# Optimization experiments

Measured on AMD Instinct MI355X. Metric: run time of the kernel, lower is better.

Reference implementation:

```python
import jax, jax.numpy as jnp
import numpy as np

HIDDEN = 1024
HEADS = 16
DEPTH = HIDDEN // HEADS  # 64
B, S = 1, 2048  # batch must be 1: E is built with shape (heads, B*S, depth) and the skew reshape assumes B*S == S


def setup_inputs() -> dict:
    key = jax.random.key(0)
    ks = jax.random.split(key, 6)
    std = 0.02
    x = jax.random.normal(ks[0], (B, S, HIDDEN), dtype=jnp.float32)
    c_attn_w = jax.random.normal(ks[1], (HIDDEN, 3 * HIDDEN), dtype=jnp.float32) * std
    c_attn_b = jnp.zeros((1, 3 * HIDDEN), dtype=jnp.float32)
    c_proj_w = jax.random.normal(ks[2], (HIDDEN, HIDDEN), dtype=jnp.float32) * std
    c_proj_b = jnp.zeros((1, HIDDEN), dtype=jnp.float32)
    # GlorotUniform for E of shape (heads, B*S, depth)
    limit = float(np.sqrt(6.0 / (B * S + DEPTH)))
    E = jax.random.uniform(ks[3], (HEADS, B * S, DEPTH), dtype=jnp.float32,
                           minval=-limit, maxval=limit)
    return {"x": x, "c_attn_w": c_attn_w, "c_attn_b": c_attn_b,
            "c_proj_w": c_proj_w, "c_proj_b": c_proj_b, "E": E}


def _split_heads(t):
    # [B,S,H] -> [B,heads,S,depth]
    b, s, h = t.shape
    return t.reshape(b, s, HEADS, h // HEADS).transpose(0, 2, 1, 3)


def _relative_attention(q, E):
    # Transformer-XL style skewing. q: [B,heads,S,depth], E: [heads,B*S,depth]
    b, h, s, d = q.shape
    q_ = q.transpose(1, 0, 2, 3).reshape(h, b * s, d)
    rel = jnp.einsum('hnd,hmd->hnm', q_, E)            # [h, B*S, B*S]
    rel = rel.reshape(h, b, s, s)
    rel = jnp.pad(rel, ((0, 0), (0, 0), (0, 0), (1, 0)))  # pad left on last dim
    rel = rel.reshape(h, b, s + 1, s)[:, :, 1:]            # skew
    return rel.transpose(1, 0, 2, 3)                       # [B,heads,S,S]


def reference(x, c_attn_w, c_attn_b, c_proj_w, c_proj_b, E):
    b, s, hidden = x.shape
    qkv = x @ c_attn_w + c_attn_b                      # [B,S,3H]
    q, k, v = jnp.split(qkv, 3, axis=2)
    q, k, v = _split_heads(q), _split_heads(k), _split_heads(v)  # [B,h,S,d]

    w = jnp.einsum('bhqd,bhkd->bhqk', q, k)            # raw scores
    w = w + _relative_attention(q, E)
    w = w * jax.lax.rsqrt(jnp.asarray(DEPTH, w.dtype))  # scale applied after rel bias

    # causal mask: 1 in lower triangle (i >= j - ns + nd, nd == ns == S)
    i = jnp.arange(s)[:, None]
    j = jnp.arange(s)[None, :]
    bmask = (i >= j).astype(w.dtype)[None, None]        # [1,1,S,S]
    w = w * bmask - 10000.0 * (1.0 - bmask)

    a = jax.nn.softmax(w, axis=-1)                      # dropout is identity at inference
    ctx = jnp.einsum('bhqk,bhkd->bhqd', a, v)
    ctx = ctx.transpose(0, 2, 1, 3).reshape(b, s, hidden)  # merge heads
    out = ctx @ c_proj_w + c_proj_b
    return out
```

## Files before the change

### kernel.cpp

```cpp
#include <hip/hip_runtime.h>
#include <math.h>

#define SEQ  2048
#define NH   16
#define DEP  64
#define HID  1024

typedef __attribute__((ext_vector_type(8))) short s16x8;
typedef __attribute__((ext_vector_type(4))) float f32x4;

#define MFMA16(a, b, c) __builtin_amdgcn_mfma_f32_16x16x32_bf16(a, b, c, 0, 0, 0)
#define GLDS16(g, l)                                                           \
  __builtin_amdgcn_global_load_lds(                                            \
      (const __attribute__((address_space(1))) void*)(g),                      \
      (__attribute__((address_space(3))) void*)(l), 16, 0, 0)

__device__ __forceinline__ ushort f2b(float f) {
  union { float f; unsigned u; } x; x.f = f;
  unsigned r = (x.u + 0x7fff + ((x.u >> 16) & 1)) >> 16;
  return (ushort)r;
}
__device__ __forceinline__ float b2f(ushort u) {
  union { unsigned u; float f; } x; x.u = ((unsigned)u) << 16;
  return x.f;
}

__global__ __launch_bounds__(256) void prep(
    const float* __restrict__ x, ushort* __restrict__ xb,
    const float* __restrict__ E, ushort* __restrict__ Eb,
    const float* __restrict__ Wa, ushort* __restrict__ Wat,
    const float* __restrict__ Wp, ushort* __restrict__ Wpt) {
  const int bid = blockIdx.x, t = threadIdx.x;
  if (bid < 1024) {
    __shared__ float Ls[64 * 68];
    const float* in; ushort* out; int C, tile;
    if (bid < 768) { in = Wa; out = Wat; C = 3072; tile = bid; }
    else           { in = Wp; out = Wpt; C = 1024; tile = bid - 768; }
    const int ntx = C / 64;
    const int n0 = (tile % ntx) * 64, k0 = (tile / ntx) * 64;
    const int r = t >> 4, c4 = t & 15;
    #pragma unroll
    for (int p = 0; p < 4; p++) {
      float4 v = *(const float4*)&in[(size_t)(k0 + r + 16 * p) * C + n0 + c4 * 4];
      *(float4*)&Ls[(r + 16 * p) * 68 + c4 * 4] = v;
    }
    __syncthreads();
    #pragma unroll
    for (int p = 0; p < 4; p++) {
      int rw = r + 16 * p;
      ushort4 o;
      o.x = f2b(Ls[(c4 * 4 + 0) * 68 + rw]);
      o.y = f2b(Ls[(c4 * 4 + 1) * 68 + rw]);
      o.z = f2b(Ls[(c4 * 4 + 2) * 68 + rw]);
      o.w = f2b(Ls[(c4 * 4 + 3) * 68 + rw]);
      *(ushort4*)&out[(size_t)(n0 + rw) * 1024 + k0 + c4 * 4] = o;
    }
  } else {
    const int id = bid - 1024;
    #pragma unroll
    for (int rep = 0; rep < 4; rep++) {
      int i = id * 256 + t + rep * 262144;
      const float* src; ushort* dst; int k;
      if (i < 524288) { src = x; dst = xb; k = i; }
      else            { src = E; dst = Eb; k = i - 524288; }
      float4 v = *(const float4*)&src[(size_t)k * 4];
      ushort4 o = {f2b(v.x), f2b(v.y), f2b(v.z), f2b(v.w)};
      *(ushort4*)&dst[(size_t)k * 4] = o;
    }
  }
}

template <int MODE>
__global__ __launch_bounds__(256, 3) void gemm_mfma(
    const ushort* __restrict__ A, const ushort* __restrict__ Bt,
    const float* __restrict__ bias, int N, int K,
    ushort* __restrict__ qd, ushort* __restrict__ kd, ushort* __restrict__ vt,
    float* __restrict__ Cout) {
  __shared__ ushort As[2][64 * 64];
  __shared__ ushort Bs[2][128 * 64];
  const int t = threadIdx.x, l = t & 63, w = t >> 6;
  const int lr = l & 15, quad = l >> 4;
  const int row8 = l >> 3;
  const int chunk = (l & 7) ^ ((l >> 3) & 7);
  const int m0 = blockIdx.y * 64, n0 = blockIdx.x * 128;
  const int wr = (w >> 1) * 32, wc = (w & 1) * 64;
  f32x4 acc[2][4] = {};
  const ushort* gA = A + (size_t)m0 * K + chunk * 8;
  const ushort* gB = Bt + (size_t)n0 * K + chunk * 8;

  auto issue = [&](int buf, int k0) {
    #pragma unroll
    for (int g = 0; g < 2; g++) {
      int r = 16 * w + 8 * g + row8;
      GLDS16(gA + (size_t)r * K + k0, &As[buf][(16 * w + 8 * g) * 64]);
    }
    #pragma unroll
    for (int g = 0; g < 4; g++) {
      int r = 32 * w + 8 * g + row8;
      GLDS16(gB + (size_t)r * K + k0, &Bs[buf][(32 * w + 8 * g) * 64]);
    }
  };

  issue(0, 0);
  const int nsteps = K / 64;
  for (int s = 0; s < nsteps; s++) {
    __syncthreads();
    if (s + 1 < nsteps) issue((s + 1) & 1, (s + 1) * 64);
    const char* as_ = (const char*)As[s & 1];
    const char* bs_ = (const char*)Bs[s & 1];
    s16x8 af[2][2], bf[4][2];
    #pragma unroll
    for (int i = 0; i < 2; i++)
      #pragma unroll
      for (int hh = 0; hh < 2; hh++)
        af[i][hh] = *(const s16x8*)(as_ + (wr + 16 * i + lr) * 128 +
                                    (((4 * hh + quad) ^ (lr & 7)) * 16));
    #pragma unroll
    for (int j = 0; j < 4; j++)
      #pragma unroll
      for (int hh = 0; hh < 2; hh++)
        bf[j][hh] = *(const s16x8*)(bs_ + (wc + 16 * j + lr) * 128 +
                                    (((4 * hh + quad) ^ (lr & 7)) * 16));
    #pragma unroll
    for (int i = 0; i < 2; i++)
      #pragma unroll
      for (int j = 0; j < 4; j++) {
        acc[i][j] = MFMA16(af[i][0], bf[j][0], acc[i][j]);
        acc[i][j] = MFMA16(af[i][1], bf[j][1], acc[i][j]);
      }
  }

  #pragma unroll
  for (int i = 0; i < 2; i++) {
    #pragma unroll
    for (int j = 0; j < 4; j++) {
      const int colg = n0 + wc + 16 * j + lr;
      const float bb = bias[colg];
      const int rowg0 = m0 + wr + 16 * i + 4 * quad;
      if (MODE == 0) {
        const int part = colg >> 10, hh = (colg >> 6) & 15, d = colg & 63;
        if (part == 2) {
          ushort4 ov;
          ov.x = f2b(acc[i][j][0] + bb);
          ov.y = f2b(acc[i][j][1] + bb);
          ov.z = f2b(acc[i][j][2] + bb);
          ov.w = f2b(acc[i][j][3] + bb);
          *(ushort4*)&vt[((size_t)hh * 64 + d) * SEQ + rowg0] = ov;
        } else {
          ushort* dst = part == 0 ? qd : kd;
          const float sc = part == 0 ? 0.125f : 1.0f;
          #pragma unroll
          for (int r = 0; r < 4; r++)
            dst[((size_t)hh * SEQ + rowg0 + r) * 64 + d] = f2b((acc[i][j][r] + bb) * sc);
        }
      } else {
        #pragma unroll
        for (int r = 0; r < 4; r++)
          Cout[(size_t)(rowg0 + r) * N + colg] = acc[i][j][r] + bb;
      }
    }
  }
}

__global__ __launch_bounds__(256, 2) void attn_mfma(
    const ushort* __restrict__ qw, const ushort* __restrict__ kw,
    const ushort* __restrict__ vT, const ushort* __restrict__ Ebf,
    ushort* __restrict__ ctx, ushort* __restrict__ pa_o,
    float* __restrict__ pa_l) {
  __shared__ ushort KT[2][64 * 64];
  __shared__ ushort VS[2][64 * 64];
  __shared__ ushort EB[2][128 * 64];
  __shared__ ushort PB[4][16 * 72];
  const int t = threadIdx.x, l = t & 63, w = t >> 6;
  const int lr = l & 15, quad = l >> 4;
  const int row8 = l >> 3;
  const int chunk = (l & 7) ^ ((l >> 3) & 7);
  const int h = blockIdx.y;
  const int p = blockIdx.x >> 1, half = blockIdx.x & 1;
  const int i0A = 64 * p, i0B = 64 * (31 - p);

  int ph_i0[2], ph_k0[2], ph_k1[2], nph, tot;
  bool ph_diag[2], ph_dir[2];
  if (half == 0) {
    ph_i0[0] = i0A; ph_k0[0] = 0; ph_k1[0] = p + 1;  ph_diag[0] = true;  ph_dir[0] = true;
    ph_i0[1] = i0B; ph_k0[1] = 0; ph_k1[1] = 16 - p; ph_diag[1] = false; ph_dir[1] = false;
    nph = 2; tot = 17;
  } else {
    ph_i0[0] = i0B; ph_k0[0] = 16 - p; ph_k1[0] = 32 - p; ph_diag[0] = true; ph_dir[0] = false;
    ph_i0[1] = 0; ph_k0[1] = 0; ph_k1[1] = 0; ph_diag[1] = false; ph_dir[1] = false;
    nph = 1; tot = 16;
  }

  const ushort* kwh = kw + (size_t)h * SEQ * 64;
  const ushort* vgh = vT + (size_t)h * 64 * SEQ;
  const ushort* egh = Ebf + (size_t)h * SEQ * 64;

  auto issue = [&](int buf, int i0_, int j0) {
    const int m0 = 1984 - i0_ + j0;
    const ushort* kb = kwh + (size_t)j0 * 64 + chunk * 8;
    const ushort* vb = vgh + j0 + chunk * 8;
    #pragma unroll
    for (int g = 0; g < 2; g++) {
      int r = 16 * w + 8 * g + row8;
      GLDS16(kb + (size_t)r * 64, &KT[buf][(16 * w + 8 * g) * 64]);
      GLDS16(vb + (size_t)r * SEQ, &VS[buf][(16 * w + 8 * g) * 64]);
    }
    #pragma unroll
    for (int g = 0; g < 4; g++) {
      int r = m0 + 32 * w + 8 * g + row8;
      if (r > SEQ - 1) r = SEQ - 1;
      GLDS16(egh + (size_t)r * 64 + chunk * 8, &EB[buf][(32 * w + 8 * g) * 64]);
    }
  };

  int pi = 0, kt = ph_k0[0];
  issue(0, ph_i0[0], kt * 64);

  s16x8 aq0, aq1;
  {
    const ushort* qg = qw + ((size_t)h * SEQ + ph_i0[0] + 16 * w) * 64;
    aq0 = *(const s16x8*)(qg + lr * 64 + quad * 8);
    aq1 = *(const s16x8*)(qg + lr * 64 + 32 + quad * 8);
  }

  f32x4 o[4] = {};
  float li[4] = {0.f, 0.f, 0.f, 0.f};
  f32x4 rtc = {};

  for (int s = 0; s < tot; s++) {
    __syncthreads();

    const int i0 = ph_i0[pi];
    const bool first = (kt == ph_k0[pi]);
    const bool last = (kt == ph_k1[pi] - 1);
    const bool diag = ph_diag[pi] && last;

    {
      int npi = pi, nkt = kt + 1;
      bool have = true;
      if (nkt == ph_k1[pi]) {
        if (pi + 1 < nph) { npi = pi + 1; nkt = ph_k0[npi]; } else have = false;
      }
      if (have) issue((s + 1) & 1, ph_i0[npi], nkt * 64);
    }

    const char* KTc = (const char*)KT[s & 1];
    const char* VSc = (const char*)VS[s & 1];
    const char* EBc = (const char*)EB[s & 1];

    f32x4 s4[4];
    #pragma unroll
    for (int b = 0; b < 4; b++) {
      const int row = 16 * b + lr;
      s16x8 bk0 = *(const s16x8*)(KTc + row * 128 + ((quad ^ (lr & 7)) * 16));
      s16x8 bk1 = *(const s16x8*)(KTc + row * 128 + (((4 + quad) ^ (lr & 7)) * 16));
      f32x4 z = {};
      z = MFMA16(aq0, bk0, z);
      z = MFMA16(aq1, bk1, z);
      s4[b] = z;
    }

    {
      const int ebase = 48 - 16 * w;
      f32x4 rt[5];
      if (first) {
        const int row = ebase + lr;
        s16x8 e0 = *(const s16x8*)(EBc + row * 128 + ((quad ^ (lr & 7)) * 16));
        s16x8 e1 = *(const s16x8*)(EBc + row * 128 + (((4 + quad) ^ (lr & 7)) * 16));
        f32x4 z = {};
        z = MFMA16(aq0, e0, z);
        z = MFMA16(aq1, e1, z);
        rt[0] = z;
      } else {
        rt[0] = rtc;
      }
      #pragma unroll
      for (int b = 1; b < 5; b++) {
        const int row = ebase + 16 * b + lr;
        s16x8 e0 = *(const s16x8*)(EBc + row * 128 + ((quad ^ (lr & 7)) * 16));
        s16x8 e1 = *(const s16x8*)(EBc + row * 128 + (((4 + quad) ^ (lr & 7)) * 16));
        f32x4 z = {};
        z = MFMA16(aq0, e0, z);
        z = MFMA16(aq1, e1, z);
        rt[b] = z;
      }
      rtc = rt[4];
      #pragma unroll
      for (int b = 0; b < 4; b++)
        #pragma unroll
        for (int r = 0; r < 4; r++) {
          int ti = 4 * quad + r;
          int u = lr - ti + 15;
          int src = (u & 15) | (l & 48);
          float v0 = __shfl(rt[b][r], src);
          float v1 = __shfl(rt[b + 1][r], src);
          s4[b][r] += (u < 16) ? v0 : v1;
        }
    }

    if (diag) {
      #pragma unroll
      for (int b = 0; b < 4; b++)
        #pragma unroll
        for (int r = 0; r < 4; r++) {
          int ii = 16 * w + 4 * quad + r;
          if (16 * b + lr > ii) s4[b][r] = -10000.0f;
        }
    }

    #pragma unroll
    for (int b = 0; b < 4; b++)
      #pragma unroll
      for (int r = 0; r < 4; r++) {
        float pp = __expf(s4[b][r]);
        s4[b][r] = pp;
        li[r] += pp;
      }

    {
      char* Pw = (char*)PB[w];
      #pragma unroll
      for (int b = 0; b < 4; b++)
        #pragma unroll
        for (int r = 0; r < 4; r++)
          *(ushort*)(Pw + (4 * quad + r) * 144 + (16 * b + lr) * 2) = f2b(s4[b][r]);
      s16x8 pa0 = *(const s16x8*)(Pw + lr * 144 + quad * 16);
      s16x8 pa1 = *(const s16x8*)(Pw + lr * 144 + 64 + quad * 16);
      #pragma unroll
      for (int dc = 0; dc < 4; dc++) {
        const int row = 16 * dc + lr;
        s16x8 bv0 = *(const s16x8*)(VSc + row * 128 + ((quad ^ (lr & 7)) * 16));
        s16x8 bv1 = *(const s16x8*)(VSc + row * 128 + (((4 + quad) ^ (lr & 7)) * 16));
        o[dc] = MFMA16(pa0, bv0, o[dc]);
        o[dc] = MFMA16(pa1, bv1, o[dc]);
      }
    }

    if (last) {
      float lsum[4];
      #pragma unroll
      for (int r = 0; r < 4; r++) {
        float v = li[r];
        v += __shfl_xor(v, 1);
        v += __shfl_xor(v, 2);
        v += __shfl_xor(v, 4);
        v += __shfl_xor(v, 8);
        lsum[r] = v;
      }
      if (ph_dir[pi]) {
        #pragma unroll
        for (int r = 0; r < 4; r++) {
          float inv = 1.0f / lsum[r];
          #pragma unroll
          for (int dc = 0; dc < 4; dc++) {
            int row = i0 + 16 * w + 4 * quad + r;
            int col = h * 64 + 16 * dc + lr;
            ctx[(size_t)row * HID + col] = f2b(o[dc][r] * inv);
          }
        }
      } else {
        ushort* po = pa_o + (((size_t)(h * 16 + p) * 2 + half) * 4096);
        float* pl = pa_l + (((size_t)(h * 16 + p) * 2 + half) * 64);
        #pragma unroll
        for (int r = 0; r < 4; r++) {
          int row = 16 * w + 4 * quad + r;
          #pragma unroll
          for (int dc = 0; dc < 4; dc++)
            po[row * 64 + 16 * dc + lr] = f2b(o[dc][r]);
          if (lr == 0) pl[row] = lsum[r];
        }
      }
      #pragma unroll
      for (int dc = 0; dc < 4; dc++) o[dc] = (f32x4){0.f, 0.f, 0.f, 0.f};
      #pragma unroll
      for (int r = 0; r < 4; r++) li[r] = 0.f;
      if (pi + 1 < nph) {
        const ushort* qg = qw + ((size_t)h * SEQ + ph_i0[pi + 1] + 16 * w) * 64;
        aq0 = *(const s16x8*)(qg + lr * 64 + quad * 8);
        aq1 = *(const s16x8*)(qg + lr * 64 + 32 + quad * 8);
      }
    }

    if (kt + 1 == ph_k1[pi]) { pi++; kt = (pi < nph) ? ph_k0[pi] : 0; }
    else kt++;
  }
}

__global__ __launch_bounds__(256) void merge_p(const ushort* __restrict__ pa_o,
                                               const float* __restrict__ pa_l,
                                               ushort* __restrict__ ctx) {
  const int p = blockIdx.x, h = blockIdx.y, t = threadIdx.x;
  const int row = t >> 2, seg = t & 3;
  const ushort* o0 = pa_o + ((size_t)(h * 16 + p) * 2 + 0) * 4096;
  const ushort* o1 = pa_o + ((size_t)(h * 16 + p) * 2 + 1) * 4096;
  const float* l0 = pa_l + ((size_t)(h * 16 + p) * 2 + 0) * 64;
  const float* l1 = pa_l + ((size_t)(h * 16 + p) * 2 + 1) * 64;
  const float inv = 1.0f / (l0[row] + l1[row]);
  const int i0b = 64 * (31 - p);
  #pragma unroll
  for (int g = 0; g < 2; g++) {
    ushort a[8], b[8], r[8];
    *(int4*)a = *(const int4*)&o0[row * 64 + seg * 16 + g * 8];
    *(int4*)b = *(const int4*)&o1[row * 64 + seg * 16 + g * 8];
    #pragma unroll
    for (int j = 0; j < 8; j++) r[j] = f2b((b2f(a[j]) + b2f(b[j])) * inv);
    *(int4*)&ctx[(size_t)(i0b + row) * HID + h * 64 + seg * 16 + g * 8] = *(int4*)r;
  }
}

extern "C" void kernel_launch(void* const* d_in, const int* in_sizes, int n_in,
                              void* d_out, int out_size, void* d_ws, size_t ws_size,
                              hipStream_t stream) {
  (void)in_sizes; (void)n_in; (void)out_size; (void)ws_size;
  const float* x  = (const float*)d_in[0];
  const float* Wa = (const float*)d_in[1];
  const float* ba = (const float*)d_in[2];
  const float* Wp = (const float*)d_in[3];
  const float* bp = (const float*)d_in[4];
  const float* E  = (const float*)d_in[5];
  float* out = (float*)d_out;

  ushort* xb  = (ushort*)d_ws;
  ushort* ctx = xb;
  ushort* Wat = xb + (size_t)2 * 1024 * 1024;
  ushort* Wpt = Wat + (size_t)3 * 1024 * 1024;
  ushort* Ebf = Wpt + (size_t)1024 * 1024;
  ushort* qwp = Ebf + (size_t)2 * 1024 * 1024;
  ushort* kwp = qwp + (size_t)2 * 1024 * 1024;
  ushort* vTp = kwp + (size_t)2 * 1024 * 1024;
  ushort* pa_o = Wat;
  float*  pa_l = (float*)(Wat + (size_t)2 * 1024 * 1024);

  prep<<<2048, 256, 0, stream>>>(x, xb, E, Ebf, Wa, Wat, Wp, Wpt);
  gemm_mfma<0><<<dim3(24, 32), 256, 0, stream>>>(xb, Wat, ba, 3 * HID, HID,
                                                 qwp, kwp, vTp, nullptr);
  attn_mfma<<<dim3(32, NH), 256, 0, stream>>>(qwp, kwp, vTp, Ebf, ctx,
                                              pa_o, pa_l);
  merge_p<<<dim3(16, NH), 256, 0, stream>>>(pa_o, pa_l, ctx);
  gemm_mfma<1><<<dim3(8, 32), 256, 0, stream>>>(ctx, Wpt, bp, HID, HID,
                                                nullptr, nullptr, nullptr, out);
}
```

Before: 158.5 us.

## Use 128-row query tiles with 4-way split-K attention and ring-buffered E rows

```diff
diff --git a/kernel.cpp b/kernel.cpp
--- a/kernel.cpp
+++ b/kernel.cpp
@@ -70,21 +70,22 @@
   }
 }
 
-template <int MODE>
+template <int MODE, int BN>
 __global__ __launch_bounds__(256, 3) void gemm_mfma(
     const ushort* __restrict__ A, const ushort* __restrict__ Bt,
     const float* __restrict__ bias, int N, int K,
     ushort* __restrict__ qd, ushort* __restrict__ kd, ushort* __restrict__ vt,
     float* __restrict__ Cout) {
+  constexpr int NJ = BN / 32;
   __shared__ ushort As[2][64 * 64];
-  __shared__ ushort Bs[2][128 * 64];
+  __shared__ ushort Bs[2][BN * 64];
   const int t = threadIdx.x, l = t & 63, w = t >> 6;
   const int lr = l & 15, quad = l >> 4;
   const int row8 = l >> 3;
   const int chunk = (l & 7) ^ ((l >> 3) & 7);
-  const int m0 = blockIdx.y * 64, n0 = blockIdx.x * 128;
-  const int wr = (w >> 1) * 32, wc = (w & 1) * 64;
-  f32x4 acc[2][4] = {};
+  const int m0 = blockIdx.y * 64, n0 = blockIdx.x * BN;
+  const int wr = (w >> 1) * 32, wc = (w & 1) * (BN / 2);
+  f32x4 acc[2][NJ] = {};
   const ushort* gA = A + (size_t)m0 * K + chunk * 8;
   const ushort* gB = Bt + (size_t)n0 * K + chunk * 8;
 
@@ -95,9 +96,9 @@
       GLDS16(gA + (size_t)r * K + k0, &As[buf][(16 * w + 8 * g) * 64]);
     }
     #pragma unroll
-    for (int g = 0; g < 4; g++) {
-      int r = 32 * w + 8 * g + row8;
-      GLDS16(gB + (size_t)r * K + k0, &Bs[buf][(32 * w + 8 * g) * 64]);
+    for (int g = 0; g < BN / 32; g++) {
+      int r = (BN / 4) * w + 8 * g + row8;
+      GLDS16(gB + (size_t)r * K + k0, &Bs[buf][((BN / 4) * w + 8 * g) * 64]);
     }
   };
 
@@ -108,7 +109,7 @@
     if (s + 1 < nsteps) issue((s + 1) & 1, (s + 1) * 64);
     const char* as_ = (const char*)As[s & 1];
     const char* bs_ = (const char*)Bs[s & 1];
-    s16x8 af[2][2], bf[4][2];
+    s16x8 af[2][2], bf[NJ][2];
     #pragma unroll
     for (int i = 0; i < 2; i++)
       #pragma unroll
@@ -116,7 +117,7 @@
         af[i][hh] = *(const s16x8*)(as_ + (wr + 16 * i + lr) * 128 +
                                     (((4 * hh + quad) ^ (lr & 7)) * 16));
     #pragma unroll
-    for (int j = 0; j < 4; j++)
+    for (int j = 0; j < NJ; j++)
       #pragma unroll
       for (int hh = 0; hh < 2; hh++)
         bf[j][hh] = *(const s16x8*)(bs_ + (wc + 16 * j + lr) * 128 +
@@ -124,7 +125,7 @@
     #pragma unroll
     for (int i = 0; i < 2; i++)
       #pragma unroll
-      for (int j = 0; j < 4; j++) {
+      for (int j = 0; j < NJ; j++) {
         acc[i][j] = MFMA16(af[i][0], bf[j][0], acc[i][j]);
         acc[i][j] = MFMA16(af[i][1], bf[j][1], acc[i][j]);
       }
@@ -133,7 +134,7 @@
   #pragma unroll
   for (int i = 0; i < 2; i++) {
     #pragma unroll
-    for (int j = 0; j < 4; j++) {
+    for (int j = 0; j < NJ; j++) {
       const int colg = n0 + wc + 16 * j + lr;
       const float bb = bias[colg];
       const int rowg0 = m0 + wr + 16 * i + 4 * quad;
@@ -165,247 +166,249 @@
 __global__ __launch_bounds__(256, 2) void attn_mfma(
     const ushort* __restrict__ qw, const ushort* __restrict__ kw,
     const ushort* __restrict__ vT, const ushort* __restrict__ Ebf,
-    ushort* __restrict__ ctx, ushort* __restrict__ pa_o,
-    float* __restrict__ pa_l) {
+    ushort* __restrict__ pa_o, float* __restrict__ pa_l) {
   __shared__ ushort KT[2][64 * 64];
   __shared__ ushort VS[2][64 * 64];
-  __shared__ ushort EB[2][128 * 64];
-  __shared__ ushort PB[4][16 * 72];
+  __shared__ ushort EB[4][64 * 64];
+  __shared__ ushort PB[4][1152];
   const int t = threadIdx.x, l = t & 63, w = t >> 6;
   const int lr = l & 15, quad = l >> 4;
   const int row8 = l >> 3;
-  const int chunk = (l & 7) ^ ((l >> 3) & 7);
+  const int chk = (l & 7) ^ ((l >> 3) & 7);
   const int h = blockIdx.y;
-  const int p = blockIdx.x >> 1, half = blockIdx.x & 1;
-  const int i0A = 64 * p, i0B = 64 * (31 - p);
-
-  int ph_i0[2], ph_k0[2], ph_k1[2], nph, tot;
-  bool ph_diag[2], ph_dir[2];
-  if (half == 0) {
-    ph_i0[0] = i0A; ph_k0[0] = 0; ph_k1[0] = p + 1;  ph_diag[0] = true;  ph_dir[0] = true;
-    ph_i0[1] = i0B; ph_k0[1] = 0; ph_k1[1] = 16 - p; ph_diag[1] = false; ph_dir[1] = false;
-    nph = 2; tot = 17;
-  } else {
-    ph_i0[0] = i0B; ph_k0[0] = 16 - p; ph_k1[0] = 32 - p; ph_diag[0] = true; ph_dir[0] = false;
-    ph_i0[1] = 0; ph_k0[1] = 0; ph_k1[1] = 0; ph_diag[1] = false; ph_dir[1] = false;
-    nph = 1; tot = 16;
-  }
+  const int pr = blockIdx.x >> 2, cid = blockIdx.x & 3;
+  const int TA = 2 * pr + 2;
+  const int s0 = (17 * cid) >> 1, s1 = (17 * (cid + 1)) >> 1;
+  const int iA = 128 * pr, iB = 128 * (15 - pr);
 
   const ushort* kwh = kw + (size_t)h * SEQ * 64;
   const ushort* vgh = vT + (size_t)h * 64 * SEQ;
   const ushort* egh = Ebf + (size_t)h * SEQ * 64;
 
-  auto issue = [&](int buf, int i0_, int j0) {
-    const int m0 = 1984 - i0_ + j0;
-    const ushort* kb = kwh + (size_t)j0 * 64 + chunk * 8;
-    const ushort* vb = vgh + j0 + chunk * 8;
+  auto issueKV = [&](int buf, int j0) {
     #pragma unroll
     for (int g = 0; g < 2; g++) {
       int r = 16 * w + 8 * g + row8;
-      GLDS16(kb + (size_t)r * 64, &KT[buf][(16 * w + 8 * g) * 64]);
-      GLDS16(vb + (size_t)r * SEQ, &VS[buf][(16 * w + 8 * g) * 64]);
-    }
-    #pragma unroll
-    for (int g = 0; g < 4; g++) {
-      int r = m0 + 32 * w + 8 * g + row8;
-      if (r > SEQ - 1) r = SEQ - 1;
-      GLDS16(egh + (size_t)r * 64 + chunk * 8, &EB[buf][(32 * w + 8 * g) * 64]);
+      GLDS16(kwh + (size_t)(j0 + r) * 64 + chk * 8, &KT[buf][(16 * w + 8 * g) * 64]);
+      GLDS16(vgh + (size_t)r * SEQ + j0 + chk * 8, &VS[buf][(16 * w + 8 * g) * 64]);
     }
   };
-
-  int pi = 0, kt = ph_k0[0];
-  issue(0, ph_i0[0], kt * 64);
-
-  s16x8 aq0, aq1;
-  {
-    const ushort* qg = qw + ((size_t)h * SEQ + ph_i0[0] + 16 * w) * 64;
-    aq0 = *(const s16x8*)(qg + lr * 64 + quad * 8);
-    aq1 = *(const s16x8*)(qg + lr * 64 + 32 + quad * 8);
-  }
-
-  f32x4 o[4] = {};
-  float li[4] = {0.f, 0.f, 0.f, 0.f};
-  f32x4 rtc = {};
-
-  for (int s = 0; s < tot; s++) {
+  auto issueE = [&](int G) {
+    const int slot = (G >> 6) & 3;
+    #pragma unroll
+    for (int g = 0; g < 2; g++) {
+      int rl = 16 * w + 8 * g + row8;
+      int grow = G + rl; if (grow > SEQ - 1) grow = SEQ - 1;
+      GLDS16(egh + (size_t)grow * 64 + chk * 8, &EB[slot][(16 * w + 8 * g) * 64]);
+    }
+  };
+  auto eread = [&](int P, int h2) -> s16x8 {
+    int rg = P + lr;
+    return *(const s16x8*)((const char*)EB + ((rg >> 6) & 3) * 8192 +
+                           (rg & 63) * 128 + (((h2 * 4 + quad) ^ (lr & 7)) * 16));
+  };
+
+  int s = s0;
+  int i0 = (s0 < TA) ? iA : iB;
+  int tau = (s0 < TA) ? pr : 15 - pr;
+  int kt = (s0 < TA) ? s0 : s0 - TA;
+
+  s16x8 aq[2][2];
+  auto loadQ = [&]() {
+    const ushort* qg = qw + ((size_t)h * SEQ + i0 + 32 * w) * 64;
+    #pragma unroll
+    for (int a = 0; a < 2; a++)
+      #pragma unroll
+      for (int h2 = 0; h2 < 2; h2++)
+        aq[a][h2] = *(const s16x8*)(qg + (16 * a + lr) * 64 + h2 * 32 + quad * 8);
+  };
+  loadQ();
+
+  int MB = 1920 - i0 + 64 * kt;
+  issueE(MB); issueE(MB + 64); issueE(MB + 128);
+  issueKV(0, 64 * kt);
+
+  f32x4 o[2][4] = {};
+  float li[2][4] = {};
+  f32x4 rt0[5], rt1[5];
+  bool first = true, efill = false;
+
+  for (; s < s1; s++) {
     __syncthreads();
-
-    const int i0 = ph_i0[pi];
-    const bool first = (kt == ph_k0[pi]);
-    const bool last = (kt == ph_k1[pi] - 1);
-    const bool diag = ph_diag[pi] && last;
-
-    {
-      int npi = pi, nkt = kt + 1;
-      bool have = true;
-      if (nkt == ph_k1[pi]) {
-        if (pi + 1 < nph) { npi = pi + 1; nkt = ph_k0[npi]; } else have = false;
-      }
-      if (have) issue((s + 1) & 1, ph_i0[npi], nkt * 64);
-    }
-
-    const char* KTc = (const char*)KT[s & 1];
-    const char* VSc = (const char*)VS[s & 1];
-    const char* EBc = (const char*)EB[s & 1];
-
-    f32x4 s4[4];
+    if (efill) {
+      issueE(MB); issueE(MB + 64); issueE(MB + 128);
+      __syncthreads();
+      efill = false;
+    }
+
+    const int j0 = 64 * kt;
+    const bool lastOfPhase = (s + 1 == TA) || (s + 1 == s1);
+    if (s + 1 < s1) {
+      if (s + 1 == TA) issueKV((s + 1 - s0) & 1, 0);
+      else { issueKV((s + 1 - s0) & 1, j0 + 64); issueE(MB + 192); }
+    }
+
+    const char* KTc = (const char*)KT[(s - s0) & 1];
+    const char* VSc = (const char*)VS[(s - s0) & 1];
+
+    f32x4 s4[2][4];
     #pragma unroll
     for (int b = 0; b < 4; b++) {
       const int row = 16 * b + lr;
       s16x8 bk0 = *(const s16x8*)(KTc + row * 128 + ((quad ^ (lr & 7)) * 16));
       s16x8 bk1 = *(const s16x8*)(KTc + row * 128 + (((4 + quad) ^ (lr & 7)) * 16));
-      f32x4 z = {};
-      z = MFMA16(aq0, bk0, z);
-      z = MFMA16(aq1, bk1, z);
-      s4[b] = z;
+      f32x4 z0 = {}, z1 = {};
+      z0 = MFMA16(aq[0][0], bk0, z0); z0 = MFMA16(aq[0][1], bk1, z0);
+      z1 = MFMA16(aq[1][0], bk0, z1); z1 = MFMA16(aq[1][1], bk1, z1);
+      s4[0][b] = z0; s4[1][b] = z1;
     }
 
     {
-      const int ebase = 48 - 16 * w;
-      f32x4 rt[5];
+      const int base = MB + 112 - 32 * w;
       if (first) {
-        const int row = ebase + lr;
-        s16x8 e0 = *(const s16x8*)(EBc + row * 128 + ((quad ^ (lr & 7)) * 16));
-        s16x8 e1 = *(const s16x8*)(EBc + row * 128 + (((4 + quad) ^ (lr & 7)) * 16));
-        f32x4 z = {};
-        z = MFMA16(aq0, e0, z);
-        z = MFMA16(aq1, e1, z);
-        rt[0] = z;
-      } else {
-        rt[0] = rtc;
-      }
-      #pragma unroll
-      for (int b = 1; b < 5; b++) {
-        const int row = ebase + 16 * b + lr;
-        s16x8 e0 = *(const s16x8*)(EBc + row * 128 + ((quad ^ (lr & 7)) * 16));
-        s16x8 e1 = *(const s16x8*)(EBc + row * 128 + (((4 + quad) ^ (lr & 7)) * 16));
-        f32x4 z = {};
-        z = MFMA16(aq0, e0, z);
-        z = MFMA16(aq1, e1, z);
-        rt[b] = z;
-      }
-      rtc = rt[4];
+        s16x8 e0 = eread(base - 16, 0), e1 = eread(base - 16, 1);
+        f32x4 z = {}; z = MFMA16(aq[1][0], e0, z); z = MFMA16(aq[1][1], e1, z);
+        rt1[0] = z;
+      } else { rt0[0] = rt0[4]; rt1[0] = rt1[4]; }
+      #pragma unroll
+      for (int m = 0; m < 5; m++) {
+        s16x8 e0 = eread(base + 16 * m, 0), e1 = eread(base + 16 * m, 1);
+        if (m >= 1) {
+          f32x4 z = {}; z = MFMA16(aq[0][0], e0, z); z = MFMA16(aq[0][1], e1, z);
+          rt0[m] = z;
+        }
+        if (m <= 3) {
+          f32x4 z = {}; z = MFMA16(aq[1][0], e0, z); z = MFMA16(aq[1][1], e1, z);
+          rt1[m + 1] = z;
+        }
+        if (first && m == 0) {
+          f32x4 z = {}; z = MFMA16(aq[0][0], e0, z); z = MFMA16(aq[0][1], e1, z);
+          rt0[0] = z;
+        }
+      }
+    }
+    #pragma unroll
+    for (int b = 0; b < 4; b++)
+      #pragma unroll
+      for (int r = 0; r < 4; r++) {
+        const int ti = 4 * quad + r;
+        const int u = lr - ti + 15;
+        const int src = (u & 15) | (l & 48);
+        float v00 = __shfl(rt0[b][r], src), v01 = __shfl(rt0[b + 1][r], src);
+        float v10 = __shfl(rt1[b][r], src), v11 = __shfl(rt1[b + 1][r], src);
+        s4[0][b][r] += (u < 16) ? v00 : v01;
+        s4[1][b][r] += (u < 16) ? v10 : v11;
+      }
+
+    #pragma unroll
+    for (int a = 0; a < 2; a++) {
+      if (j0 + 63 > i0 + 32 * w + 16 * a) {
+        #pragma unroll
+        for (int b = 0; b < 4; b++)
+          #pragma unroll
+          for (int r = 0; r < 4; r++) {
+            int ii = i0 + 32 * w + 16 * a + 4 * quad + r;
+            int jj = j0 + 16 * b + lr;
+            if (jj > ii) s4[a][b][r] = -10000.0f;
+          }
+      }
+    }
+
+    #pragma unroll
+    for (int a = 0; a < 2; a++)
       #pragma unroll
       for (int b = 0; b < 4; b++)
         #pragma unroll
         for (int r = 0; r < 4; r++) {
-          int ti = 4 * quad + r;
-          int u = lr - ti + 15;
-          int src = (u & 15) | (l & 48);
-          float v0 = __shfl(rt[b][r], src);
-          float v1 = __shfl(rt[b + 1][r], src);
-          s4[b][r] += (u < 16) ? v0 : v1;
-        }
-    }
-
-    if (diag) {
-      #pragma unroll
-      for (int b = 0; b < 4; b++)
-        #pragma unroll
-        for (int r = 0; r < 4; r++) {
-          int ii = 16 * w + 4 * quad + r;
-          if (16 * b + lr > ii) s4[b][r] = -10000.0f;
-        }
-    }
-
-    #pragma unroll
-    for (int b = 0; b < 4; b++)
-      #pragma unroll
-      for (int r = 0; r < 4; r++) {
-        float pp = __expf(s4[b][r]);
-        s4[b][r] = pp;
-        li[r] += pp;
-      }
-
-    {
-      char* Pw = (char*)PB[w];
-      #pragma unroll
-      for (int b = 0; b < 4; b++)
-        #pragma unroll
-        for (int r = 0; r < 4; r++)
-          *(ushort*)(Pw + (4 * quad + r) * 144 + (16 * b + lr) * 2) = f2b(s4[b][r]);
-      s16x8 pa0 = *(const s16x8*)(Pw + lr * 144 + quad * 16);
-      s16x8 pa1 = *(const s16x8*)(Pw + lr * 144 + 64 + quad * 16);
+          float pp = __expf(s4[a][b][r]);
+          s4[a][b][r] = pp;
+          li[a][r] += pp;
+        }
+
+    char* Pw = (char*)PB + w * 2304;
+    #pragma unroll
+    for (int hc = 0; hc < 2; hc++) {
+      #pragma unroll
+      for (int a = 0; a < 2; a++)
+        #pragma unroll
+        for (int bb = 0; bb < 2; bb++)
+          #pragma unroll
+          for (int r = 0; r < 4; r++)
+            *(ushort*)(Pw + (16 * a + 4 * quad + r) * 72 + (16 * bb + lr) * 2) =
+                f2b(s4[a][2 * hc + bb][r]);
+      s16x8 pa0 = *(const s16x8*)(Pw + lr * 72 + quad * 16);
+      s16x8 pa1 = *(const s16x8*)(Pw + (16 + lr) * 72 + quad * 16);
       #pragma unroll
       for (int dc = 0; dc < 4; dc++) {
         const int row = 16 * dc + lr;
-        s16x8 bv0 = *(const s16x8*)(VSc + row * 128 + ((quad ^ (lr & 7)) * 16));
-        s16x8 bv1 = *(const s16x8*)(VSc + row * 128 + (((4 + quad) ^ (lr & 7)) * 16));
-        o[dc] = MFMA16(pa0, bv0, o[dc]);
-        o[dc] = MFMA16(pa1, bv1, o[dc]);
-      }
-    }
-
-    if (last) {
-      float lsum[4];
-      #pragma unroll
-      for (int r = 0; r < 4; r++) {
-        float v = li[r];
-        v += __shfl_xor(v, 1);
-        v += __shfl_xor(v, 2);
-        v += __shfl_xor(v, 4);
-        v += __shfl_xor(v, 8);
-        lsum[r] = v;
-      }
-      if (ph_dir[pi]) {
+        s16x8 bv = *(const s16x8*)(VSc + row * 128 + (((hc * 4 + quad) ^ (lr & 7)) * 16));
+        o[0][dc] = MFMA16(pa0, bv, o[0][dc]);
+        o[1][dc] = MFMA16(pa1, bv, o[1][dc]);
+      }
+    }
+
+    if (lastOfPhase) {
+      ushort* po = pa_o + (size_t)((h * 16 + tau) * 4 + cid) * 8192;
+      float* pl = pa_l + (size_t)((h * 16 + tau) * 4 + cid) * 128;
+      #pragma unroll
+      for (int a = 0; a < 2; a++)
         #pragma unroll
         for (int r = 0; r < 4; r++) {
-          float inv = 1.0f / lsum[r];
-          #pragma unroll
-          for (int dc = 0; dc < 4; dc++) {
-            int row = i0 + 16 * w + 4 * quad + r;
-            int col = h * 64 + 16 * dc + lr;
-            ctx[(size_t)row * HID + col] = f2b(o[dc][r] * inv);
-          }
-        }
-      } else {
-        ushort* po = pa_o + (((size_t)(h * 16 + p) * 2 + half) * 4096);
-        float* pl = pa_l + (((size_t)(h * 16 + p) * 2 + half) * 64);
-        #pragma unroll
-        for (int r = 0; r < 4; r++) {
-          int row = 16 * w + 4 * quad + r;
+          float v = li[a][r];
+          v += __shfl_xor(v, 1); v += __shfl_xor(v, 2);
+          v += __shfl_xor(v, 4); v += __shfl_xor(v, 8);
+          const int row = 32 * w + 16 * a + 4 * quad + r;
+          if (lr == 0) pl[row] = v;
           #pragma unroll
           for (int dc = 0; dc < 4; dc++)
-            po[row * 64 + 16 * dc + lr] = f2b(o[dc][r]);
-          if (lr == 0) pl[row] = lsum[r];
-        }
-      }
-      #pragma unroll
-      for (int dc = 0; dc < 4; dc++) o[dc] = (f32x4){0.f, 0.f, 0.f, 0.f};
-      #pragma unroll
-      for (int r = 0; r < 4; r++) li[r] = 0.f;
-      if (pi + 1 < nph) {
-        const ushort* qg = qw + ((size_t)h * SEQ + ph_i0[pi + 1] + 16 * w) * 64;
-        aq0 = *(const s16x8*)(qg + lr * 64 + quad * 8);
-        aq1 = *(const s16x8*)(qg + lr * 64 + 32 + quad * 8);
-      }
-    }
-
-    if (kt + 1 == ph_k1[pi]) { pi++; kt = (pi < nph) ? ph_k0[pi] : 0; }
-    else kt++;
+            po[row * 64 + 16 * dc + lr] = f2b(o[a][dc][r]);
+          li[a][r] = 0.f;
+        }
+      #pragma unroll
+      for (int a = 0; a < 2; a++)
+        #pragma unroll
+        for (int dc = 0; dc < 4; dc++) o[a][dc] = (f32x4){0.f, 0.f, 0.f, 0.f};
+    }
+
+    if (s + 1 == TA && s + 1 < s1) {
+      i0 = iB; tau = 15 - pr; kt = 0; MB = 1920 - iB;
+      loadQ(); first = true; efill = true;
+    } else { kt++; MB += 64; first = false; }
   }
 }
 
 __global__ __launch_bounds__(256) void merge_p(const ushort* __restrict__ pa_o,
                                                const float* __restrict__ pa_l,
                                                ushort* __restrict__ ctx) {
-  const int p = blockIdx.x, h = blockIdx.y, t = threadIdx.x;
-  const int row = t >> 2, seg = t & 3;
-  const ushort* o0 = pa_o + ((size_t)(h * 16 + p) * 2 + 0) * 4096;
-  const ushort* o1 = pa_o + ((size_t)(h * 16 + p) * 2 + 1) * 4096;
-  const float* l0 = pa_l + ((size_t)(h * 16 + p) * 2 + 0) * 64;
-  const float* l1 = pa_l + ((size_t)(h * 16 + p) * 2 + 1) * 64;
-  const float inv = 1.0f / (l0[row] + l1[row]);
-  const int i0b = 64 * (31 - p);
+  const int tau = blockIdx.x, h = blockIdx.y, t = threadIdx.x;
+  const int row = t >> 1, chf = t & 1;
+  const int pr = (tau < 8) ? tau : 15 - tau;
+  const int TA = 2 * pr + 2;
+  float acc[32] = {};
+  float lsum = 0.f;
   #pragma unroll
-  for (int g = 0; g < 2; g++) {
-    ushort a[8], b[8], r[8];
-    *(int4*)a = *(const int4*)&o0[row * 64 + seg * 16 + g * 8];
-    *(int4*)b = *(const int4*)&o1[row * 64 + seg * 16 + g * 8];
-    #pragma unroll
-    for (int j = 0; j < 8; j++) r[j] = f2b((b2f(a[j]) + b2f(b[j])) * inv);
-    *(int4*)&ctx[(size_t)(i0b + row) * HID + h * 64 + seg * 16 + g * 8] = *(int4*)r;
+  for (int c = 0; c < 4; c++) {
+    bool cov = (tau < 8) ? (((17 * c) >> 1) < TA) : (((17 * (c + 1)) >> 1) > TA);
+    if (cov) {
+      const size_t base = (size_t)((h * 16 + tau) * 4 + c);
+      lsum += pa_l[base * 128 + row];
+      const ushort* po = pa_o + base * 8192 + row * 64 + chf * 32;
+      #pragma unroll
+      for (int g = 0; g < 4; g++) {
+        ushort tmp[8];
+        *(int4*)tmp = *(const int4*)(po + g * 8);
+        #pragma unroll
+        for (int j = 0; j < 8; j++) acc[g * 8 + j] += b2f(tmp[j]);
+      }
+    }
   }
+  const float inv = 1.0f / lsum;
+  ushort outv[32];
+  #pragma unroll
+  for (int j = 0; j < 32; j++) outv[j] = f2b(acc[j] * inv);
+  ushort* cp = ctx + (size_t)(tau * 128 + row) * HID + h * 64 + chf * 32;
+  #pragma unroll
+  for (int g = 0; g < 4; g++) *(int4*)(cp + g * 8) = *(int4*)&outv[g * 8];
 }
 
 extern "C" void kernel_launch(void* const* d_in, const int* in_sizes, int n_in,
@@ -428,15 +431,14 @@
   ushort* qwp = Ebf + (size_t)2 * 1024 * 1024;
   ushort* kwp = qwp + (size_t)2 * 1024 * 1024;
   ushort* vTp = kwp + (size_t)2 * 1024 * 1024;
-  ushort* pa_o = Wat;
-  float*  pa_l = (float*)(Wat + (size_t)2 * 1024 * 1024);
+  ushort* pa_o = vTp + (size_t)2 * 1024 * 1024;
+  float*  pa_l = (float*)(pa_o + (size_t)8 * 1024 * 1024);
 
   prep<<<2048, 256, 0, stream>>>(x, xb, E, Ebf, Wa, Wat, Wp, Wpt);
-  gemm_mfma<0><<<dim3(24, 32), 256, 0, stream>>>(xb, Wat, ba, 3 * HID, HID,
-                                                 qwp, kwp, vTp, nullptr);
-  attn_mfma<<<dim3(32, NH), 256, 0, stream>>>(qwp, kwp, vTp, Ebf, ctx,
-                                              pa_o, pa_l);
+  gemm_mfma<0, 128><<<dim3(24, 32), 256, 0, stream>>>(xb, Wat, ba, 3 * HID, HID,
+                                                      qwp, kwp, vTp, nullptr);
+  attn_mfma<<<dim3(32, NH), 256, 0, stream>>>(qwp, kwp, vTp, Ebf, pa_o, pa_l);
   merge_p<<<dim3(16, NH), 256, 0, stream>>>(pa_o, pa_l, ctx);
-  gemm_mfma<1><<<dim3(8, 32), 256, 0, stream>>>(ctx, Wpt, bp, HID, HID,
-                                                nullptr, nullptr, nullptr, out);
-}
+  gemm_mfma<1, 64><<<dim3(16, 32), 256, 0, stream>>>(ctx, Wpt, bp, HID, HID,
+                                                     nullptr, nullptr, nullptr, out);
+}
```

After: 164.2 us. 1.04x slower.
